# Kernel tuning notes

Hardware: AMD Instinct MI355X
Metric: run time of the kernel (lower is better)

The kernel has to match this reference:

```python
import jax, jax.numpy as jnp
import numpy as np

NUM_BINS = 256          # CLAHE histogram bins (kornia default)
GRID = (8, 8)           # CLAHE tile grid (kornia default)
LOG_GAIN = 2.5          # module init arg
CLIP_LIMIT = 1.0        # module init arg


def normalize_in_range(x, lo=0.0, hi=1.0):
    mn = x.min()
    mx = x.max()
    return (x - mn) / (mx - mn) * (hi - lo) + lo


def adjust_log(x, gain):
    # skimage/kornia log adjust: gain * log2(1 + x)
    return gain * jnp.log2(1.0 + x)


def equalize_clahe(x, clip_limit=CLIP_LIMIT, grid=GRID):
    B, C, H, W = x.shape
    gh, gw = grid
    th = -(-H // gh)   # ceil tile height
    tw = -(-W // gw)   # ceil tile width
    Hp, Wp = th * gh, tw * gw
    if (Hp, Wp) != (H, W):
        x = jnp.pad(x, ((0, 0), (0, 0), (0, Hp - H), (0, Wp - W)), mode='reflect')

    # bin index per pixel (values saturated into [0,1])
    xc = jnp.clip(x, 0.0, 1.0)
    bins = jnp.clip((xc * NUM_BINS).astype(jnp.int32), 0, NUM_BINS - 1)  # B,C,Hp,Wp

    # --- per-tile histograms: (B*C*gh*gw) tiles of th*tw pixels ---
    tb = bins.reshape(B, C, gh, th, gw, tw).transpose(0, 1, 2, 4, 3, 5)
    tb = tb.reshape(B * C * gh * gw, th * tw)
    hist = jax.vmap(lambda ix: jnp.bincount(ix, length=NUM_BINS))(tb).astype(jnp.float32)

    pixels = th * tw
    # --- clip + uniform redistribution of excess ---
    if clip_limit > 0:
        clip_max = max(int(clip_limit * pixels // NUM_BINS), 1)
        excess = jnp.maximum(hist - clip_max, 0.0).sum(-1)
        hist = jnp.minimum(hist, float(clip_max))
        redist = jnp.floor(excess / NUM_BINS)
        residual = excess - redist * NUM_BINS
        hist = hist + redist[:, None] \
             + (jnp.arange(NUM_BINS)[None, :] < residual[:, None]).astype(hist.dtype)

    # --- CDF -> LUT in [0, 255] ---
    lut = jnp.clip(jnp.floor(jnp.cumsum(hist, -1) * ((NUM_BINS - 1) / pixels)), 0.0, NUM_BINS - 1.0)
    lut = lut.reshape(B, C, gh, gw, NUM_BINS)

    # --- bilinear interpolation between the 4 neighboring tile LUTs ---
    iy = jnp.arange(Hp, dtype=jnp.float32)
    ty = (iy + 0.5) / th - 0.5
    y0f = jnp.floor(ty)
    wy = (ty - y0f)[:, None]                                   # Hp x 1
    y0 = jnp.clip(y0f.astype(jnp.int32), 0, gh - 1)[:, None]
    y1 = jnp.clip(y0f.astype(jnp.int32) + 1, 0, gh - 1)[:, None]

    ix = jnp.arange(Wp, dtype=jnp.float32)
    tx = (ix + 0.5) / tw - 0.5
    x0f = jnp.floor(tx)
    wx = (tx - x0f)[None, :]
    x0 = jnp.clip(x0f.astype(jnp.int32), 0, gw - 1)[None, :]
    x1 = jnp.clip(x0f.astype(jnp.int32) + 1, 0, gw - 1)[None, :]

    flat_lut = lut.reshape(-1)
    bidx = jnp.arange(B)[:, None, None, None]
    cidx = jnp.arange(C)[None, :, None, None]

    def gather(yi, xi):
        idx = (((bidx * C + cidx) * gh + yi) * gw + xi) * NUM_BINS + bins
        return flat_lut[idx]

    v = (1.0 - wy) * ((1.0 - wx) * gather(y0, x0) + wx * gather(y0, x1)) \
        + wy * ((1.0 - wx) * gather(y1, x0) + wx * gather(y1, x1))
    out = v / (NUM_BINS - 1)
    return out[..., :H, :W]


def setup_inputs() -> dict:
    key = jax.random.key(0)
    x = jax.random.uniform(key, (8, 1, 2048, 2048), dtype=jnp.float32)
    return {"x": x}


def reference(x):
    shape = x.shape
    x = normalize_in_range(x, 0.0, 1.0)
    x = adjust_log(x, gain=LOG_GAIN)
    x = equalize_clahe(x, clip_limit=CLIP_LIMIT)
    x = normalize_in_range(x, 0.0, 1.0)
    return x.reshape(shape)
```

## Files before the change

kernel.cpp:

```cpp
#include <hip/hip_runtime.h>

#define NIMG 8
#define IMH 2048
#define IMW 2048
#define GH 8
#define GW 8
#define NBINS 256
#define NTPI 64
#define CLIP_MAXF 256.0f
#define LUT_SCALE 0.0038909912109375f
#define LOG_GAIN_F 2.5f

#define MM_BLOCKS 2048
#define APPLY_BLOCKS (16 * 16 * NIMG)

__device__ __forceinline__ int pix_bin(float v, float mn, float den) {
    float xn = (v - mn) / den;
    float t  = LOG_GAIN_F * log2f(1.0f + xn);
    float xc = fminf(fmaxf(t, 0.0f), 1.0f);
    int b = (int)(xc * 256.0f);
    return min(max(b, 0), 255);
}

__device__ __forceinline__ void mm4(float4 v, float& mn, float& mx) {
    mn = fminf(mn, fminf(fminf(v.x, v.y), fminf(v.z, v.w)));
    mx = fmaxf(mx, fmaxf(fmaxf(v.x, v.y), fmaxf(v.z, v.w)));
}

template <int NWAVES>
__device__ __forceinline__ void block_minmax_all(float& mn, float& mx, int t) {
#pragma unroll
    for (int m = 32; m >= 1; m >>= 1) {
        mn = fminf(mn, __shfl_xor(mn, m, 64));
        mx = fmaxf(mx, __shfl_xor(mx, m, 64));
    }
    __shared__ float smn[NWAVES], smx[NWAVES];
    int wid = t >> 6, lid = t & 63;
    if (lid == 0) { smn[wid] = mn; smx[wid] = mx; }
    __syncthreads();
    mn = smn[0]; mx = smx[0];
#pragma unroll
    for (int i = 1; i < NWAVES; i++) { mn = fminf(mn, smn[i]); mx = fmaxf(mx, smx[i]); }
}

__global__ __launch_bounds__(256) void k_minmax_in(const float4* __restrict__ x,
                                                   float2* __restrict__ red) {
    int t = threadIdx.x;
    size_t base = (size_t)blockIdx.x * 4096 + t;
    float mn = 3.4e38f, mx = -3.4e38f;
#pragma unroll
    for (int k = 0; k < 16; k += 4) {
        float4 v0 = x[base + (size_t)(k + 0) * 256];
        float4 v1 = x[base + (size_t)(k + 1) * 256];
        float4 v2 = x[base + (size_t)(k + 2) * 256];
        float4 v3 = x[base + (size_t)(k + 3) * 256];
        mm4(v0, mn, mx); mm4(v1, mn, mx); mm4(v2, mn, mx); mm4(v3, mn, mx);
    }
    block_minmax_all<4>(mn, mx, t);
    if (t == 0) red[blockIdx.x] = make_float2(mn, mx);
}

__global__ __launch_bounds__(256) void k_reduce_minmax(const float2* __restrict__ red, int n,
                                                       float* __restrict__ sc, int slot) {
    int t = threadIdx.x;
    float mn = 3.4e38f, mx = -3.4e38f;
    for (int i = t; i < n; i += 256) {
        float2 p = red[i];
        mn = fminf(mn, p.x);
        mx = fmaxf(mx, p.y);
    }
    block_minmax_all<4>(mn, mx, t);
    if (t == 0) { sc[slot] = mn; sc[slot + 1] = mx; }
}

template <bool STOREBINS>
__global__ __launch_bounds__(1024) void k_hist(const float* __restrict__ x,
                                               const float2* __restrict__ red1,
                                               float* __restrict__ lut,
                                               uchar4* __restrict__ bins) {
    int t = threadIdx.x;

    float mn, mx;
    {
        float2 p0 = red1[t];
        float2 p1 = red1[t + 1024];
        mn = fminf(p0.x, p1.x);
        mx = fmaxf(p0.y, p1.y);
        block_minmax_all<16>(mn, mx, t);
    }
    float den = mx - mn;

    __shared__ unsigned sh[NBINS];
    if (t < NBINS) sh[t] = 0u;
    __syncthreads();

    int tile = blockIdx.x;
    int img  = blockIdx.y;
    int ty = tile >> 3, tx = tile & 7;

    size_t base = ((size_t)img * IMH + (size_t)ty * 256) * IMW + (size_t)tx * 256;
    const float* xt = x + base;
    int lid = t & 63;
    int rowoff = t >> 6;
    int c4 = t & 63;

    for (int it = 0; it < 16; ++it) {
        int r = (it << 4) + rowoff;
        float4 v = *(const float4*)(xt + (size_t)r * IMW + (c4 << 2));
        int b[4];
        b[0] = pix_bin(v.x, mn, den);
        b[1] = pix_bin(v.y, mn, den);
        b[2] = pix_bin(v.z, mn, den);
        b[3] = pix_bin(v.w, mn, den);
#pragma unroll
        for (int j = 0; j < 4; j++) {
            bool hot = (b[j] == 255);
            unsigned long long m = __ballot(hot);
            if (!hot) atomicAdd(&sh[b[j]], 1u);
            if (lid == 0 && m) atomicAdd(&sh[255], (unsigned)__popcll(m));
        }
        if (STOREBINS) {
            uchar4 q;
            q.x = (unsigned char)b[0]; q.y = (unsigned char)b[1];
            q.z = (unsigned char)b[2]; q.w = (unsigned char)b[3];
            bins[(base + (size_t)r * IMW + (size_t)(c4 << 2)) >> 2] = q;
        }
    }
    __syncthreads();

    int wid = t >> 6;
    float h = 0.0f, ex = 0.0f;
    if (t < NBINS) {
        h = (float)sh[t];
        ex = fmaxf(h - CLIP_MAXF, 0.0f);
    }
    float s = ex;
#pragma unroll
    for (int m = 1; m < 64; m <<= 1) s += __shfl_xor(s, m, 64);
    __shared__ float wpart[16];
    if (lid == 0) wpart[wid] = s;
    __syncthreads();
    float excess = wpart[0] + wpart[1] + wpart[2] + wpart[3];

    h = fminf(h, CLIP_MAXF);
    float redist   = floorf(excess * (1.0f / 256.0f));
    float residual = excess - redist * 256.0f;
    h = h + redist + (((float)t < residual) ? 1.0f : 0.0f);

    float c = h;
#pragma unroll
    for (int m = 1; m < 64; m <<= 1) {
        float o = __shfl_up(c, m, 64);
        if (lid >= m) c += o;
    }
    __shared__ float wsum[16];
    if (lid == 63) wsum[wid] = c;
    __syncthreads();
    if (t < NBINS) {
        float off = 0.0f;
        for (int i = 0; i < wid; i++) off += wsum[i];
        c += off;
        float l = fminf(floorf(c * LUT_SCALE), 255.0f);
        l = fmaxf(l, 0.0f);
        lut[((size_t)img * NTPI + tile) * NBINS + t] = l;
    }
}

template <bool USE_BINS, bool FINAL>
__global__ __launch_bounds__(256) void k_apply(const uchar4* __restrict__ bins,
                                               const float* __restrict__ x,
                                               const float* __restrict__ lut,
                                               const float* __restrict__ sc,
                                               float2* __restrict__ red2,
                                               float4* __restrict__ out) {
    __shared__ float L[4][NBINS];
    int t = threadIdx.x;

    float pmn = 0.f, oscale = 1.f;
    if (FINAL) {
        float vmn = 3.4e38f, vmx = -3.4e38f;
#pragma unroll
        for (int k = 0; k < 8; k++) {
            float2 p = red2[t + k * 256];
            vmn = fminf(vmn, p.x);
            vmx = fmaxf(vmx, p.y);
        }
        block_minmax_all<4>(vmn, vmx, t);
        pmn = vmn * (1.0f / 255.0f);
        float pmx = vmx * (1.0f / 255.0f);
        oscale = 1.0f / (pmx - pmn);
    }

    int qx = blockIdx.x, qy = blockIdx.y, img = blockIdx.z;
    int ty = qy >> 1, tx = qx >> 1;
    int yA = (qy & 1) ? ty : max(ty - 1, 0);
    int yB = (qy & 1) ? min(ty + 1, GH - 1) : ty;
    int xA = (qx & 1) ? tx : max(tx - 1, 0);
    int xB = (qx & 1) ? min(tx + 1, GW - 1) : tx;

    const float* lb = lut + (size_t)img * NTPI * NBINS;
    L[0][t] = lb[(size_t)(yA * GW + xA) * NBINS + t];
    L[1][t] = lb[(size_t)(yA * GW + xB) * NBINS + t];
    L[2][t] = lb[(size_t)(yB * GW + xA) * NBINS + t];
    L[3][t] = lb[(size_t)(yB * GW + xB) * NBINS + t];
    __syncthreads();

    float mn = 0.f, den = 1.f;
    if (!USE_BINS) { mn = sc[0]; den = sc[1] - mn; }

    float vmnl = 3.4e38f, vmxl = -3.4e38f;
    int gy0 = qy << 7, gx0 = qx << 7;
    int rowoff = t >> 5;
    int c4 = t & 31;

    for (int it = 0; it < 16; ++it) {
        int r = (it << 3) + rowoff;
        int iy = gy0 + r;
        int ix0 = gx0 + (c4 << 2);
        size_t pidx = ((size_t)img * IMH + iy) * IMW + ix0;

        int b[4];
        if (USE_BINS) {
            uchar4 q = bins[pidx >> 2];
            b[0] = q.x; b[1] = q.y; b[2] = q.z; b[3] = q.w;
        } else {
            float4 v = *(const float4*)(x + pidx);
            b[0] = pix_bin(v.x, mn, den);
            b[1] = pix_bin(v.y, mn, den);
            b[2] = pix_bin(v.z, mn, den);
            b[3] = pix_bin(v.w, mn, den);
        }

        float tyf = ((float)iy + 0.5f) * (1.0f / 256.0f) - 0.5f;
        float wy = tyf - floorf(tyf);
        float4 o;
        float* op = &o.x;
#pragma unroll
        for (int j = 0; j < 4; j++) {
            float txf = ((float)(ix0 + j) + 0.5f) * (1.0f / 256.0f) - 0.5f;
            float wx = txf - floorf(txf);
            float g00 = L[0][b[j]], g01 = L[1][b[j]];
            float g10 = L[2][b[j]], g11 = L[3][b[j]];
            float v = (1.0f - wy) * ((1.0f - wx) * g00 + wx * g01) +
                      wy * ((1.0f - wx) * g10 + wx * g11);
            if (FINAL) {
                float p = v * (1.0f / 255.0f);
                op[j] = (p - pmn) * oscale;
            } else {
                vmnl = fminf(vmnl, v);
                vmxl = fmaxf(vmxl, v);
            }
        }
        if (FINAL) out[pidx >> 2] = o;
    }

    if (!FINAL) {
        block_minmax_all<4>(vmnl, vmxl, t);
        if (t == 0) {
            int bid = (img * 16 + qy) * 16 + qx;
            red2[bid] = make_float2(vmnl, vmxl);
        }
    }
}

extern "C" void kernel_launch(void* const* d_in, const int* in_sizes, int n_in,
                              void* d_out, int out_size, void* d_ws, size_t ws_size,
                              hipStream_t stream) {
    const float* x = (const float*)d_in[0];
    float4* out = (float4*)d_out;

    unsigned char* ws = (unsigned char*)d_ws;
    float* sc     = (float*)ws;
    float* lut    = (float*)(ws + 64);
    float2* red1  = (float2*)(ws + 64 + 512 * 1024);
    float2* red2  = (float2*)(ws + 64 + 512 * 1024 + 16384);
    uchar4* bins  = (uchar4*)(ws + 1024 * 1024);

    size_t need_bins = 1024 * 1024 + (size_t)NIMG * IMH * IMW;
    bool use_bins = (ws_size >= need_bins);

    k_minmax_in<<<dim3(MM_BLOCKS), dim3(256), 0, stream>>>((const float4*)x, red1);

    dim3 qgrid(16, 16, NIMG);
    if (use_bins) {
        k_hist<true><<<dim3(NTPI, NIMG), dim3(1024), 0, stream>>>(x, red1, lut, bins);
        k_apply<true, false><<<qgrid, dim3(256), 0, stream>>>(bins, x, lut, sc, red2, out);
        k_apply<true, true><<<qgrid, dim3(256), 0, stream>>>(bins, x, lut, sc, red2, out);
    } else {
        k_reduce_minmax<<<dim3(1), dim3(256), 0, stream>>>(red1, MM_BLOCKS, sc, 0);
        k_hist<false><<<dim3(NTPI, NIMG), dim3(1024), 0, stream>>>(x, red1, lut, bins);
        k_apply<false, false><<<qgrid, dim3(256), 0, stream>>>(bins, x, lut, sc, red2, out);
        k_apply<false, true><<<qgrid, dim3(256), 0, stream>>>(bins, x, lut, sc, red2, out);
    }
}
```

Before: 121.4 us.

## Pack four tile LUTs as float4, use nontemporal output stores, drop fallback path

```diff
diff --git a/kernel.cpp b/kernel.cpp
--- a/kernel.cpp
+++ b/kernel.cpp
@@ -14,6 +14,8 @@
 #define MM_BLOCKS 2048
 #define APPLY_BLOCKS (16 * 16 * NIMG)
 
+typedef float f32x4 __attribute__((ext_vector_type(4)));
+
 __device__ __forceinline__ int pix_bin(float v, float mn, float den) {
     float xn = (v - mn) / den;
     float t  = LOG_GAIN_F * log2f(1.0f + xn);
@@ -47,33 +49,24 @@
                                                    float2* __restrict__ red) {
     int t = threadIdx.x;
     size_t base = (size_t)blockIdx.x * 4096 + t;
-    float mn = 3.4e38f, mx = -3.4e38f;
+    float mn0 = 3.4e38f, mx0 = -3.4e38f;
+    float mn1 = 3.4e38f, mx1 = -3.4e38f;
+    float mn2 = 3.4e38f, mx2 = -3.4e38f;
+    float mn3 = 3.4e38f, mx3 = -3.4e38f;
 #pragma unroll
     for (int k = 0; k < 16; k += 4) {
         float4 v0 = x[base + (size_t)(k + 0) * 256];
         float4 v1 = x[base + (size_t)(k + 1) * 256];
         float4 v2 = x[base + (size_t)(k + 2) * 256];
         float4 v3 = x[base + (size_t)(k + 3) * 256];
-        mm4(v0, mn, mx); mm4(v1, mn, mx); mm4(v2, mn, mx); mm4(v3, mn, mx);
-    }
+        mm4(v0, mn0, mx0); mm4(v1, mn1, mx1); mm4(v2, mn2, mx2); mm4(v3, mn3, mx3);
+    }
+    float mn = fminf(fminf(mn0, mn1), fminf(mn2, mn3));
+    float mx = fmaxf(fmaxf(mx0, mx1), fmaxf(mx2, mx3));
     block_minmax_all<4>(mn, mx, t);
     if (t == 0) red[blockIdx.x] = make_float2(mn, mx);
 }
 
-__global__ __launch_bounds__(256) void k_reduce_minmax(const float2* __restrict__ red, int n,
-                                                       float* __restrict__ sc, int slot) {
-    int t = threadIdx.x;
-    float mn = 3.4e38f, mx = -3.4e38f;
-    for (int i = t; i < n; i += 256) {
-        float2 p = red[i];
-        mn = fminf(mn, p.x);
-        mx = fmaxf(mx, p.y);
-    }
-    block_minmax_all<4>(mn, mx, t);
-    if (t == 0) { sc[slot] = mn; sc[slot + 1] = mx; }
-}
-
-template <bool STOREBINS>
 __global__ __launch_bounds__(1024) void k_hist(const float* __restrict__ x,
                                                const float2* __restrict__ red1,
                                                float* __restrict__ lut,
@@ -119,12 +112,10 @@
             if (!hot) atomicAdd(&sh[b[j]], 1u);
             if (lid == 0 && m) atomicAdd(&sh[255], (unsigned)__popcll(m));
         }
-        if (STOREBINS) {
-            uchar4 q;
-            q.x = (unsigned char)b[0]; q.y = (unsigned char)b[1];
-            q.z = (unsigned char)b[2]; q.w = (unsigned char)b[3];
-            bins[(base + (size_t)r * IMW + (size_t)(c4 << 2)) >> 2] = q;
-        }
+        uchar4 q;
+        q.x = (unsigned char)b[0]; q.y = (unsigned char)b[1];
+        q.z = (unsigned char)b[2]; q.w = (unsigned char)b[3];
+        bins[(base + (size_t)r * IMW + (size_t)(c4 << 2)) >> 2] = q;
     }
     __syncthreads();
 
@@ -166,14 +157,12 @@
     }
 }
 
-template <bool USE_BINS, bool FINAL>
+template <bool FINAL>
 __global__ __launch_bounds__(256) void k_apply(const uchar4* __restrict__ bins,
-                                               const float* __restrict__ x,
                                                const float* __restrict__ lut,
-                                               const float* __restrict__ sc,
                                                float2* __restrict__ red2,
                                                float4* __restrict__ out) {
-    __shared__ float L[4][NBINS];
+    __shared__ float4 Lq[NBINS];
     int t = threadIdx.x;
 
     float pmn = 0.f, oscale = 1.f;
@@ -192,21 +181,21 @@
     }
 
     int qx = blockIdx.x, qy = blockIdx.y, img = blockIdx.z;
-    int ty = qy >> 1, tx = qx >> 1;
-    int yA = (qy & 1) ? ty : max(ty - 1, 0);
-    int yB = (qy & 1) ? min(ty + 1, GH - 1) : ty;
-    int xA = (qx & 1) ? tx : max(tx - 1, 0);
-    int xB = (qx & 1) ? min(tx + 1, GW - 1) : tx;
-
     const float* lb = lut + (size_t)img * NTPI * NBINS;
-    L[0][t] = lb[(size_t)(yA * GW + xA) * NBINS + t];
-    L[1][t] = lb[(size_t)(yA * GW + xB) * NBINS + t];
-    L[2][t] = lb[(size_t)(yB * GW + xA) * NBINS + t];
-    L[3][t] = lb[(size_t)(yB * GW + xB) * NBINS + t];
-    __syncthreads();
-
-    float mn = 0.f, den = 1.f;
-    if (!USE_BINS) { mn = sc[0]; den = sc[1] - mn; }
+    {
+        int ty2 = qy >> 1, tx2 = qx >> 1;
+        int yA = (qy & 1) ? ty2 : max(ty2 - 1, 0);
+        int yB = (qy & 1) ? min(ty2 + 1, GH - 1) : ty2;
+        int xA = (qx & 1) ? tx2 : max(tx2 - 1, 0);
+        int xB = (qx & 1) ? min(tx2 + 1, GW - 1) : tx2;
+        float4 g;
+        g.x = lb[(size_t)(yA * GW + xA) * NBINS + t];
+        g.y = lb[(size_t)(yA * GW + xB) * NBINS + t];
+        g.z = lb[(size_t)(yB * GW + xA) * NBINS + t];
+        g.w = lb[(size_t)(yB * GW + xB) * NBINS + t];
+        Lq[t] = g;
+    }
+    __syncthreads();
 
     float vmnl = 3.4e38f, vmxl = -3.4e38f;
     int gy0 = qy << 7, gx0 = qx << 7;
@@ -218,18 +207,8 @@
         int iy = gy0 + r;
         int ix0 = gx0 + (c4 << 2);
         size_t pidx = ((size_t)img * IMH + iy) * IMW + ix0;
-
-        int b[4];
-        if (USE_BINS) {
-            uchar4 q = bins[pidx >> 2];
-            b[0] = q.x; b[1] = q.y; b[2] = q.z; b[3] = q.w;
-        } else {
-            float4 v = *(const float4*)(x + pidx);
-            b[0] = pix_bin(v.x, mn, den);
-            b[1] = pix_bin(v.y, mn, den);
-            b[2] = pix_bin(v.z, mn, den);
-            b[3] = pix_bin(v.w, mn, den);
-        }
+        uchar4 q = bins[pidx >> 2];
+        int b[4] = {q.x, q.y, q.z, q.w};
 
         float tyf = ((float)iy + 0.5f) * (1.0f / 256.0f) - 0.5f;
         float wy = tyf - floorf(tyf);
@@ -239,10 +218,9 @@
         for (int j = 0; j < 4; j++) {
             float txf = ((float)(ix0 + j) + 0.5f) * (1.0f / 256.0f) - 0.5f;
             float wx = txf - floorf(txf);
-            float g00 = L[0][b[j]], g01 = L[1][b[j]];
-            float g10 = L[2][b[j]], g11 = L[3][b[j]];
-            float v = (1.0f - wy) * ((1.0f - wx) * g00 + wx * g01) +
-                      wy * ((1.0f - wx) * g10 + wx * g11);
+            float4 g = Lq[b[j]];
+            float v = (1.0f - wy) * ((1.0f - wx) * g.x + wx * g.y) +
+                      wy * ((1.0f - wx) * g.z + wx * g.w);
             if (FINAL) {
                 float p = v * (1.0f / 255.0f);
                 op[j] = (p - pmn) * oscale;
@@ -251,7 +229,10 @@
                 vmxl = fmaxf(vmxl, v);
             }
         }
-        if (FINAL) out[pidx >> 2] = o;
+        if (FINAL) {
+            f32x4 ov = {o.x, o.y, o.z, o.w};
+            __builtin_nontemporal_store(ov, (f32x4*)&out[pidx >> 2]);
+        }
     }
 
     if (!FINAL) {
@@ -270,26 +251,14 @@
     float4* out = (float4*)d_out;
 
     unsigned char* ws = (unsigned char*)d_ws;
-    float* sc     = (float*)ws;
     float* lut    = (float*)(ws + 64);
     float2* red1  = (float2*)(ws + 64 + 512 * 1024);
     float2* red2  = (float2*)(ws + 64 + 512 * 1024 + 16384);
     uchar4* bins  = (uchar4*)(ws + 1024 * 1024);
 
-    size_t need_bins = 1024 * 1024 + (size_t)NIMG * IMH * IMW;
-    bool use_bins = (ws_size >= need_bins);
-
     k_minmax_in<<<dim3(MM_BLOCKS), dim3(256), 0, stream>>>((const float4*)x, red1);
-
+    k_hist<<<dim3(NTPI, NIMG), dim3(1024), 0, stream>>>(x, red1, lut, bins);
     dim3 qgrid(16, 16, NIMG);
-    if (use_bins) {
-        k_hist<true><<<dim3(NTPI, NIMG), dim3(1024), 0, stream>>>(x, red1, lut, bins);
-        k_apply<true, false><<<qgrid, dim3(256), 0, stream>>>(bins, x, lut, sc, red2, out);
-        k_apply<true, true><<<qgrid, dim3(256), 0, stream>>>(bins, x, lut, sc, red2, out);
-    } else {
-        k_reduce_minmax<<<dim3(1), dim3(256), 0, stream>>>(red1, MM_BLOCKS, sc, 0);
-        k_hist<false><<<dim3(NTPI, NIMG), dim3(1024), 0, stream>>>(x, red1, lut, bins);
-        k_apply<false, false><<<qgrid, dim3(256), 0, stream>>>(bins, x, lut, sc, red2, out);
-        k_apply<false, true><<<qgrid, dim3(256), 0, stream>>>(bins, x, lut, sc, red2, out);
-    }
-}
+    k_apply<false><<<qgrid, dim3(256), 0, stream>>>(bins, lut, red2, out);
+    k_apply<true><<<qgrid, dim3(256), 0, stream>>>(bins, lut, red2, out);
+}
```

After: 113.5 us. -6.5%, faster.
